# Kernel tuning notes

Hardware: AMD Instinct MI355X
Metric: run time of the kernel (lower is better)

## Reference

```python
import jax, jax.numpy as jnp
import numpy as np

B, S, D, H = 2, 2048, 1024, 16
HD = D // H  # head_dim = 64


def setup_inputs() -> dict:
    key = jax.random.key(0)
    ks = jax.random.split(key, 6)
    scale = 0.02
    x = jax.random.normal(ks[0], (B, S, D), dtype=jnp.float32)
    Wq = jax.random.normal(ks[1], (D, D), dtype=jnp.float32) * scale
    Wk = jax.random.normal(ks[2], (D, D), dtype=jnp.float32) * scale
    Wv = jax.random.normal(ks[3], (D, D), dtype=jnp.float32) * scale
    Wo = jax.random.normal(ks[4], (D, D), dtype=jnp.float32) * scale
    bo = jnp.zeros((D,), dtype=jnp.float32)
    return {"x": x, "Wq": Wq, "Wk": Wk, "Wv": Wv, "Wo": Wo, "bo": bo}


def reference(x, Wq, Wk, Wv, Wo, bo):
    b, s, _ = x.shape
    # Linear projections (qkv_bias=False), split into heads: [b, h, s, hd]
    def split_heads(t):
        return t.reshape(b, s, H, HD).transpose(0, 2, 1, 3)
    q = split_heads(x @ Wq)
    k = split_heads(x @ Wk)
    v = split_heads(x @ Wv)
    # Scaled dot-product scores: [b, h, s, s]
    scores = jnp.einsum('bhqd,bhkd->bhqk', q, k) / jnp.sqrt(jnp.float32(HD))
    # Causal mask: triu(ones, diagonal=1) positions -> -inf
    causal = jnp.triu(jnp.ones((s, s), dtype=bool), k=1)
    scores = jnp.where(causal, -jnp.inf, scores)
    attn = jax.nn.softmax(scores, axis=-1)
    # dropout p=0.0 (eval-equivalent): identity
    ctx = jnp.einsum('bhqk,bhkd->bhqd', attn, v)  # [b, h, s, hd]
    ctx = ctx.transpose(0, 2, 1, 3).reshape(b, s, D)
    return ctx @ Wo + bo
```

## Files before the change

kernel.cpp:

```cpp
#include <hip/hip_runtime.h>
#include <math.h>

#define BB 2
#define SS 2048
#define DD 1024
#define HH 16
#define HD 64
#define MM (BB * SS)

typedef __bf16 bf16;
typedef __attribute__((ext_vector_type(8))) __bf16 bf16x8;
typedef __attribute__((ext_vector_type(4))) __bf16 bf16x4;
typedef __attribute__((ext_vector_type(4))) short short4v;
typedef __attribute__((ext_vector_type(4))) float f32x4;

#if __has_builtin(__builtin_amdgcn_exp2f)
#define EXP2F(x) __builtin_amdgcn_exp2f(x)
#else
#define EXP2F(x) exp2f(x)
#endif

__device__ __forceinline__ f32x4 pv_mfma16(bf16x4 a, short4v b, f32x4 c) {
    return __builtin_amdgcn_mfma_f32_16x16x16bf16_1k(
        __builtin_bit_cast(short4v, a), b, c, 0, 0, 0);
}

__device__ __forceinline__ void gld_lds16(const void* g, void* l) {
    __builtin_amdgcn_global_load_lds(
        (const __attribute__((address_space(1))) void*)g,
        (__attribute__((address_space(3))) void*)l, 16, 0, 0);
}

__global__ __launch_bounds__(256) void prep(
    const float* __restrict__ x,
    const float* __restrict__ W0, const float* __restrict__ W1,
    const float* __restrict__ W2, const float* __restrict__ W3,
    bf16* __restrict__ xb, bf16* __restrict__ Wt)
{
    __shared__ float tile[32][33];
    const int z = blockIdx.z;
    if (z < 4) {
        const float* W = (z == 0) ? W0 : (z == 1) ? W1 : (z == 2) ? W2 : W3;
        bf16* O = Wt + (size_t)z * DD * DD;
        const int tx = threadIdx.x & 31, ty = threadIdx.x >> 5;
        const int k0 = blockIdx.y * 32, n0 = blockIdx.x * 32;
#pragma unroll
        for (int i = 0; i < 4; ++i)
            tile[ty + i * 8][tx] = W[(size_t)(k0 + ty + i * 8) * DD + n0 + tx];
        __syncthreads();
#pragma unroll
        for (int i = 0; i < 4; ++i)
            O[(size_t)(n0 + ty + i * 8) * DD + k0 + tx] = (bf16)tile[tx][ty + i * 8];
    } else {
        const int lb = (z - 4) * 1024 + blockIdx.y * 32 + blockIdx.x;
        const size_t i = ((size_t)lb * 256 + threadIdx.x) * 8;
        const float4 a = *(const float4*)(x + i);
        const float4 b = *(const float4*)(x + i + 4);
        bf16x8 o;
        o[0] = (bf16)a.x; o[1] = (bf16)a.y; o[2] = (bf16)a.z; o[3] = (bf16)a.w;
        o[4] = (bf16)b.x; o[5] = (bf16)b.y; o[6] = (bf16)b.z; o[7] = (bf16)b.w;
        *(bf16x8*)(xb + i) = o;
    }
}

template <int SWAP>
__device__ __forceinline__ void mfma_core(
    const bf16* __restrict__ A, const bf16* __restrict__ Bt,
    int bm, int bn, int K, bf16* As, bf16* Bs, f32x4 (&acc)[4][4])
{
    const int t = threadIdx.x;
    const int w = t >> 6;
    const int l16 = t & 15, quad = (t >> 4) & 3;
    const int wr = w >> 1, wc = w & 1;
    const int arow = t >> 2;
    const int achk = (((t & 3) ^ ((t >> 3) & 3)) << 3);

    const bf16* gA = A + (size_t)(bm + arow) * K + achk;
    const bf16* gB = Bt + (size_t)(bn + arow) * K + achk;
    bf16* lA = As + w * 512;
    bf16* lB = Bs + w * 512;

    const int swz = (l16 >> 1) & 3;
    int offA[4], offB[4];
#pragma unroll
    for (int i = 0; i < 4; ++i) {
        offA[i] = (wr * 64 + i * 16 + l16) * 32 + ((quad ^ swz) << 3);
        offB[i] = (wc * 64 + i * 16 + l16) * 32 + ((quad ^ swz) << 3);
    }

#define GSTAGE(BUF, KO) do {                                                  \
        gld_lds16(gA + (KO),                  lA + (BUF) * 4096);             \
        gld_lds16(gA + (size_t)64 * K + (KO), lA + (BUF) * 4096 + 2048);      \
        gld_lds16(gB + (KO),                  lB + (BUF) * 4096);             \
        gld_lds16(gB + (size_t)64 * K + (KO), lB + (BUF) * 4096 + 2048);      \
    } while (0)

#define GCOMPUTE(BUF) do {                                                    \
        const bf16* Ab = As + (BUF) * 4096;                                   \
        const bf16* Bb = Bs + (BUF) * 4096;                                   \
        bf16x8 af[4], bv[4];                                                  \
        _Pragma("unroll")                                                     \
        for (int i = 0; i < 4; ++i) {                                         \
            af[i] = *(const bf16x8*)(Ab + offA[i]);                           \
            bv[i] = *(const bf16x8*)(Bb + offB[i]);                           \
        }                                                                     \
        _Pragma("unroll")                                                     \
        for (int mi = 0; mi < 4; ++mi)                                        \
            _Pragma("unroll")                                                 \
            for (int ni = 0; ni < 4; ++ni)                                    \
                acc[mi][ni] = SWAP                                            \
                    ? __builtin_amdgcn_mfma_f32_16x16x32_bf16(                \
                          bv[ni], af[mi], acc[mi][ni], 0, 0, 0)               \
                    : __builtin_amdgcn_mfma_f32_16x16x32_bf16(                \
                          af[mi], bv[ni], acc[mi][ni], 0, 0, 0);              \
    } while (0)

#define GBAR() do {                                                           \
        asm volatile("s_barrier" ::: "memory");                               \
        __builtin_amdgcn_sched_barrier(0);                                    \
    } while (0)

    GSTAGE(0, 0);
    const int nk = K >> 5;
    for (int kt = 0; kt < nk; kt += 2) {
        GSTAGE(1, (kt + 1) << 5);
        asm volatile("s_waitcnt vmcnt(4)" ::: "memory");
        GBAR();
        GCOMPUTE(0);
        asm volatile("s_waitcnt lgkmcnt(0)" ::: "memory");
        GBAR();
        if (kt + 2 < nk) {
            GSTAGE(0, (kt + 2) << 5);
            asm volatile("s_waitcnt vmcnt(4)" ::: "memory");
        } else {
            asm volatile("s_waitcnt vmcnt(0)" ::: "memory");
        }
        GBAR();
        GCOMPUTE(1);
        asm volatile("s_waitcnt lgkmcnt(0)" ::: "memory");
        GBAR();
    }
#undef GBAR
#undef GCOMPUTE
#undef GSTAGE
}

__global__ __launch_bounds__(256) void gemm_qkv(
    const bf16* __restrict__ xb, const bf16* __restrict__ Wt,
    bf16* __restrict__ Qb, bf16* __restrict__ Kb, bf16* __restrict__ Vb)
{
    __shared__ __align__(16) bf16 As[2 * 128 * 32];
    __shared__ __align__(16) bf16 Bs[2 * 128 * 32];

    const int lin = blockIdx.x + (blockIdx.y << 3) + (blockIdx.z << 8);
    const int wrk = (lin & 7) * 96 + (lin >> 3);
    const int bn = (wrk & 7) * 128;
    const int bm = ((wrk >> 3) & 31) * 128;
    const int z  = wrk >> 8;

    const int t = threadIdx.x;
    const int w = t >> 6, l16 = t & 15, quad = (t >> 4) & 3;
    const int wr = w >> 1, wc = w & 1;

    f32x4 acc[4][4] = {};
    if (z < 2) {
        mfma_core<1>(xb, Wt + (size_t)z * DD * DD, bm, bn, DD, As, Bs, acc);
        bf16* outp = (z == 0) ? Qb : Kb;
        const float scl = (z == 0) ? 0.18033688011f : 1.0f;
#pragma unroll
        for (int mi = 0; mi < 4; ++mi) {
            const int srow = bm + wr * 64 + mi * 16 + l16;
            const int b = srow >> 11, s = srow & (SS - 1);
#pragma unroll
            for (int ni = 0; ni < 4; ++ni) {
                const int colb = bn + wc * 64 + ni * 16 + quad * 4;
                const int h = colb >> 6, hd = colb & 63;
                bf16x4 o;
#pragma unroll
                for (int r = 0; r < 4; ++r) o[r] = (bf16)(acc[mi][ni][r] * scl);
                *(bf16x4*)(outp + ((size_t)((b * HH + h) * SS + s)) * HD + hd) = o;
            }
        }
    } else {
        mfma_core<0>(xb, Wt + (size_t)2 * DD * DD, bm, bn, DD, As, Bs, acc);
#pragma unroll
        for (int mi = 0; mi < 4; ++mi) {
            const int srow0 = bm + wr * 64 + mi * 16 + quad * 4;
            const int b = srow0 >> 11, s0 = srow0 & (SS - 1);
#pragma unroll
            for (int ni = 0; ni < 4; ++ni) {
                const int col = bn + wc * 64 + ni * 16 + l16;
                const int h = col >> 6, hd = col & 63;
                bf16x4 o;
#pragma unroll
                for (int r = 0; r < 4; ++r) o[r] = (bf16)acc[mi][ni][r];
                *(bf16x4*)(Vb + ((size_t)((b * HH + h) * HD + hd)) * SS + s0) = o;
            }
        }
    }
}

__global__ __launch_bounds__(256) void gemm_out(
    const bf16* __restrict__ ctx, const bf16* __restrict__ Wto,
    const float* __restrict__ bias, float* __restrict__ out)
{
    __shared__ __align__(16) bf16 As[2 * 128 * 32];
    __shared__ __align__(16) bf16 Bs[2 * 128 * 32];

    const int lin = blockIdx.x + (blockIdx.y << 3);
    const int wrk = (lin & 7) * 32 + (lin >> 3);
    const int bn = (wrk & 7) * 128;
    const int bm = (wrk >> 3) * 128;

    f32x4 acc[4][4] = {};
    mfma_core<1>(ctx, Wto, bm, bn, DD, As, Bs, acc);

    const int t = threadIdx.x;
    const int w = t >> 6, l16 = t & 15, quad = (t >> 4) & 3;
    const int wr = w >> 1, wc = w & 1;

#pragma unroll
    for (int mi = 0; mi < 4; ++mi) {
        const int row = bm + wr * 64 + mi * 16 + l16;
#pragma unroll
        for (int ni = 0; ni < 4; ++ni) {
            const int colb = bn + wc * 64 + ni * 16 + quad * 4;
            const float4 b4 = *(const float4*)(bias + colb);
            float4 o;
            o.x = acc[mi][ni][0] + b4.x;
            o.y = acc[mi][ni][1] + b4.y;
            o.z = acc[mi][ni][2] + b4.z;
            o.w = acc[mi][ni][3] + b4.w;
            *(float4*)(out + (size_t)row * DD + colb) = o;
        }
    }
}

__global__ __launch_bounds__(512, 4) void attn_flash(
    const bf16* __restrict__ Q, const bf16* __restrict__ K,
    const bf16* __restrict__ Vt, bf16* __restrict__ ctx)
{
    __shared__ __align__(16) bf16 Ks[2][64 * 64];
    __shared__ __align__(16) bf16 Vs[2][64 * 64];

    const int t = threadIdx.x;
    const int w = t >> 6;
    const int lane = t & 63;
    const int l16 = lane & 15, quad = lane >> 4;

    const int L  = blockIdx.x;
    const int bh = L & 31;
    const int slot = L >> 5;
    const int g = (slot < 8) ? 15 - slot : slot - 8;
    const int q0b = g * 128;
    const int q0w = q0b + w * 16;
    const int qrow = q0w + l16;
    const int nkt = 2 * g + 2;

    const bf16* Qp = Q  + ((size_t)bh * SS + q0w) * HD;
    const bf16* Kp = K  + (size_t)bh * SS * HD;
    const bf16* Vp = Vt + (size_t)bh * HD * SS;

    const bf16x8 bQ0 = *(const bf16x8*)(Qp + l16 * HD + quad * 8);
    const bf16x8 bQ1 = *(const bf16x8*)(Qp + l16 * HD + 32 + quad * 8);

    const int srow = w * 8 + (lane >> 3);
    const int c = ((lane & 7) - srow) & 7;
    const bf16* gK = Kp + (size_t)srow * HD + c * 8;
    const bf16* gV = Vp + (size_t)srow * SS + c * 8;
    bf16* const lK = &Ks[0][w * 512];
    bf16* const lV = &Vs[0][w * 512];

#define STAGE(BUF, KB) do {                                              \
        gld_lds16(gK + (size_t)(KB) * HD, lK + (BUF) * 4096);            \
        gld_lds16(gV + (KB),              lV + (BUF) * 4096);            \
    } while (0)

    const int offK0 = l16 * 64 + ((quad + l16) & 7) * 8;
    const int offK1 = l16 * 64 + ((quad + 4 + l16) & 7) * 8;
    int offV[4];
#pragma unroll
    for (int mi = 0; mi < 4; ++mi)
        offV[mi] = l16 * 64 + ((((quad >> 1) + 2 * mi + l16) & 7) * 8)
                 + (quad & 1) * 4;

    const bf16* const KsB = &Ks[0][0];
    const bf16* const VsB = &Vs[0][0];

    f32x4 accO[4] = {{0,0,0,0},{0,0,0,0},{0,0,0,0},{0,0,0,0}};
    float Lr = 0.f;

#define TILE(BUF, KB) do {                                                   \
        f32x4 St[4] = {{0,0,0,0},{0,0,0,0},{0,0,0,0},{0,0,0,0}};             \
        __builtin_amdgcn_s_setprio(1);                                       \
        _Pragma("unroll")                                                    \
        for (int mi = 0; mi < 4; ++mi) {                                     \
            const bf16x8 a0 = *(const bf16x8*)(KsB + (BUF) * 4096            \
                                               + mi * 1024 + offK0);         \
            const bf16x8 a1 = *(const bf16x8*)(KsB + (BUF) * 4096            \
                                               + mi * 1024 + offK1);         \
            St[mi] = __builtin_amdgcn_mfma_f32_16x16x32_bf16(                \
                a0, bQ0, St[mi], 0, 0, 0);                                   \
            St[mi] = __builtin_amdgcn_mfma_f32_16x16x32_bf16(                \
                a1, bQ1, St[mi], 0, 0, 0);                                   \
        }                                                                    \
        __builtin_amdgcn_s_setprio(0);                                       \
        if ((KB) + 63 > q0w) {                                               \
            _Pragma("unroll")                                                \
            for (int mi = 0; mi < 4; ++mi)                                   \
                _Pragma("unroll")                                            \
                for (int rr = 0; rr < 4; ++rr)                               \
                    if ((KB) + mi * 16 + quad * 4 + rr > qrow)               \
                        St[mi][rr] = -1e30f;                                 \
        }                                                                    \
        float rs = 0.f;                                                      \
        short4v pb[4];                                                       \
        _Pragma("unroll")                                                    \
        for (int mi = 0; mi < 4; ++mi) {                                     \
            bf16x4 pk;                                                       \
            _Pragma("unroll")                                                \
            for (int rr = 0; rr < 4; ++rr) {                                 \
                const float p = EXP2F(St[mi][rr]);                           \
                rs += p;                                                     \
                pk[rr] = (bf16)p;                                            \
            }                                                                \
            pb[mi] = __builtin_bit_cast(short4v, pk);                        \
        }                                                                    \
        rs += __shfl_xor(rs, 16);                                            \
        rs += __shfl_xor(rs, 32);                                            \
        Lr += rs;                                                            \
        __builtin_amdgcn_s_setprio(1);                                       \
        _Pragma("unroll")                                                    \
        for (int mi = 0; mi < 4; ++mi) {                                     \
            _Pragma("unroll")                                                 \
            for (int db = 0; db < 4; ++db) {                                 \
                const bf16x4 aV = *(const bf16x4*)(VsB + (BUF) * 4096        \
                                                   + db * 1024 + offV[mi]);  \
                accO[db] = pv_mfma16(aV, pb[mi], accO[db]);                  \
            }                                                                \
        }                                                                    \
        __builtin_amdgcn_s_setprio(0);                                       \
    } while (0)

    STAGE(0, 0);
    int kb = 0;
    for (int kt = 0; kt < nkt; kt += 2) {
        __syncthreads();
        STAGE(1, kb + 64);
        TILE(0, kb);
        __syncthreads();
        if (kt + 2 < nkt) {
            STAGE(0, kb + 128);
            TILE(1, kb + 64);
        } else {
            if (w >= 4) TILE(1, kb + 64);
        }
        kb += 128;
    }
#undef TILE
#undef STAGE

    const float rinv = 1.0f / Lr;
    const int b = bh >> 4, h = bh & (HH - 1);
    bf16* op = ctx + ((size_t)(b * SS + q0w + l16)) * DD + h * HD;
#pragma unroll
    for (int db = 0; db < 4; ++db) {
        bf16x4 o;
#pragma unroll
        for (int rr = 0; rr < 4; ++rr) o[rr] = (bf16)(accO[db][rr] * rinv);
        *(bf16x4*)(op + db * 16 + quad * 4) = o;
    }
}

extern "C" void kernel_launch(void* const* d_in, const int* in_sizes, int n_in,
                              void* d_out, int out_size, void* d_ws, size_t ws_size,
                              hipStream_t stream)
{
    const float* x  = (const float*)d_in[0];
    const float* Wq = (const float*)d_in[1];
    const float* Wk = (const float*)d_in[2];
    const float* Wv = (const float*)d_in[3];
    const float* Wo = (const float*)d_in[4];
    const float* bo = (const float*)d_in[5];
    float* out = (float*)d_out;

    const size_t chunk = (size_t)MM * DD;
    bf16* xb  = (bf16*)d_ws;
    bf16* Wt  = xb + chunk;
    bf16* Qb  = Wt + 4 * (size_t)DD * DD;
    bf16* Kb  = Qb + chunk;
    bf16* Vb  = Kb + chunk;
    bf16* ctx = Vb + chunk;

    prep<<<dim3(32, 32, 6), dim3(256), 0, stream>>>(x, Wq, Wk, Wv, Wo, xb, Wt);

    gemm_qkv<<<dim3(DD / 128, MM / 128, 3), dim3(256), 0, stream>>>(xb, Wt, Qb, Kb, Vb);

    attn_flash<<<dim3(BB * HH * (SS / 128)), dim3(512), 0, stream>>>(Qb, Kb, Vb, ctx);

    gemm_out<<<dim3(DD / 128, MM / 128), dim3(256), 0, stream>>>(
        ctx, Wt + 3 * (size_t)DD * DD, bo, out);
}
```

Measured before the change: 178.9 us.

## Triple-buffer K/V tiles in flash attention with explicit vmcnt waits

Switches the attention kernel's K/V shared-memory staging from double to triple buffering, keeping two tile loads in flight. It replaces two __syncthreads per pair of tiles with one s_waitcnt vmcnt plus s_barrier per tile, so compute on the current tile overlaps with loads two tiles ahead. The cost is 16 KB more LDS per block, which may lower occupancy, and a reliance on hand-written waitcnt counts that must match the number of outstanding async loads.

Result: slower. 185.3 us (+3.6%).

```diff
diff --git a/kernel.cpp b/kernel.cpp
--- a/kernel.cpp
+++ b/kernel.cpp
@@ -240,8 +240,8 @@
     const bf16* __restrict__ Q, const bf16* __restrict__ K,
     const bf16* __restrict__ Vt, bf16* __restrict__ ctx)
 {
-    __shared__ __align__(16) bf16 Ks[2][64 * 64];
-    __shared__ __align__(16) bf16 Vs[2][64 * 64];
+    __shared__ __align__(16) bf16 Ks[3][64 * 64];
+    __shared__ __align__(16) bf16 Vs[3][64 * 64];
 
     const int t = threadIdx.x;
     const int w = t >> 6;
@@ -271,9 +271,9 @@
     bf16* const lK = &Ks[0][w * 512];
     bf16* const lV = &Vs[0][w * 512];
 
-#define STAGE(BUF, KB) do {                                              \
-        gld_lds16(gK + (size_t)(KB) * HD, lK + (BUF) * 4096);            \
-        gld_lds16(gV + (KB),              lV + (BUF) * 4096);            \
+#define STAGE(SB, KB) do {                                               \
+        gld_lds16(gK + (size_t)(KB) * HD, lK + (SB));                    \
+        gld_lds16(gV + (KB),              lV + (SB));                    \
     } while (0)
 
     const int offK0 = l16 * 64 + ((quad + l16) & 7) * 8;
@@ -290,14 +290,14 @@
     f32x4 accO[4] = {{0,0,0,0},{0,0,0,0},{0,0,0,0},{0,0,0,0}};
     float Lr = 0.f;
 
-#define TILE(BUF, KB) do {                                                   \
+#define TILE(VB, KB) do {                                                    \
         f32x4 St[4] = {{0,0,0,0},{0,0,0,0},{0,0,0,0},{0,0,0,0}};             \
         __builtin_amdgcn_s_setprio(1);                                       \
         _Pragma("unroll")                                                    \
         for (int mi = 0; mi < 4; ++mi) {                                     \
-            const bf16x8 a0 = *(const bf16x8*)(KsB + (BUF) * 4096            \
+            const bf16x8 a0 = *(const bf16x8*)(KsB + (VB)                    \
                                                + mi * 1024 + offK0);         \
-            const bf16x8 a1 = *(const bf16x8*)(KsB + (BUF) * 4096            \
+            const bf16x8 a1 = *(const bf16x8*)(KsB + (VB)                    \
                                                + mi * 1024 + offK1);         \
             St[mi] = __builtin_amdgcn_mfma_f32_16x16x32_bf16(                \
                 a0, bQ0, St[mi], 0, 0, 0);                                   \
@@ -334,7 +334,7 @@
         for (int mi = 0; mi < 4; ++mi) {                                     \
             _Pragma("unroll")                                                 \
             for (int db = 0; db < 4; ++db) {                                 \
-                const bf16x4 aV = *(const bf16x4*)(VsB + (BUF) * 4096        \
+                const bf16x4 aV = *(const bf16x4*)(VsB + (VB)                \
                                                    + db * 1024 + offV[mi]);  \
                 accO[db] = pv_mfma16(aV, pb[mi], accO[db]);                  \
             }                                                                \
@@ -343,19 +343,24 @@
     } while (0)
 
     STAGE(0, 0);
+    STAGE(4096, 64);
+
+    int vb = 0;
+    int sb = 8192;
     int kb = 0;
-    for (int kt = 0; kt < nkt; kt += 2) {
-        __syncthreads();
-        STAGE(1, kb + 64);
-        TILE(0, kb);
-        __syncthreads();
-        if (kt + 2 < nkt) {
-            STAGE(0, kb + 128);
-            TILE(1, kb + 64);
+    for (int kt = 0; kt < nkt; ++kt) {
+        if (kt + 1 < nkt) {
+            asm volatile("s_waitcnt vmcnt(2)" ::: "memory");
         } else {
-            if (w >= 4) TILE(1, kb + 64);
+            asm volatile("s_waitcnt vmcnt(0)" ::: "memory");
         }
-        kb += 128;
+        asm volatile("s_barrier" ::: "memory");
+        __builtin_amdgcn_sched_barrier(0);
+        if (kt + 2 < nkt) STAGE(sb, kb + 128);
+        if (kt + 1 < nkt || w >= 4) TILE(vb, kb);
+        kb += 64;
+        vb = (vb == 8192) ? 0 : vb + 4096;
+        sb = (sb == 8192) ? 0 : sb + 4096;
     }
 #undef TILE
 #undef STAGE
```
